# Optimization experiments

Hardware: AMD Instinct MI355X
Metric: run time of the kernel (lower is better)

## Reference

```python
import jax, jax.numpy as jnp
import numpy as np

IN_F = (16, 16, 16)
OUT_F = (16, 16, 16)
RANKS = (8, 8, 8, 8, 8, 8)


def setup_inputs() -> dict:
    key = jax.random.key(0)
    ks = jax.random.split(key, 9)
    x = jax.random.normal(ks[0], (4096, int(np.prod(IN_F))), dtype=jnp.float32)
    # core ~ U[0,1)*0.1 as in torch.rand(ranks)*0.1
    core = jax.random.uniform(ks[1], RANKS, dtype=jnp.float32) * 0.1
    # factor matrices: 3 out-side (out_f[i], r[i]) then 3 in-side (in_f[i], r[i+3])
    shapes = [(OUT_F[i], RANKS[i]) for i in range(3)] + [(IN_F[i], RANKS[i + 3]) for i in range(3)]
    f0, f1, f2, f3, f4, f5 = [
        jax.random.normal(ks[2 + i], shapes[i], dtype=jnp.float32) * 0.1 for i in range(6)
    ]
    bias = jnp.zeros((int(np.prod(OUT_F)),), dtype=jnp.float32)
    return {"x": x, "core": core, "f0": f0, "f1": f1, "f2": f2,
            "f3": f3, "f4": f4, "f5": f5, "bias": bias}


def reference(x, core, f0, f1, f2, f3, f4, f5, bias):
    # x: [N, prod(IN_F)] -> [N, i1, i2, i3]
    xr = x.reshape(-1, *IN_F)
    # Reconstruct full dense weight from Tucker factors (faithful to original)
    # core: [r0..r5]; f0..f2 out-side (out_dim, r); f3..f5 in-side (in_dim, r)
    W = jnp.einsum('ijklmn,ai,bj,ck,dl,em,fn->abcdef', core, f0, f1, f2, f3, f4, f5)
    # Contract input with in-side modes: [N, o1, o2, o3]
    res = jnp.einsum('abcdef,ndef->nabc', W, xr)
    y = res.reshape(-1, int(np.prod(OUT_F)))
    return y + bias
```

## Files before the change

kernel.cpp:

```cpp
#include <hip/hip_runtime.h>

#define THREADS 256

typedef __attribute__((ext_vector_type(8))) short bf16x8;
typedef __attribute__((ext_vector_type(4))) float f32x4;

__device__ inline unsigned short f2bf(float f) {
    union { float f; unsigned int u; } v; v.f = f;
    unsigned int r = v.u + 0x7fffu + ((v.u >> 16) & 1u);
    return (unsigned short)(r >> 16);
}

__global__ __launch_bounds__(THREADS) void k_in_contract(
    const float* __restrict__ x,
    const float* __restrict__ f3, const float* __restrict__ f4,
    const float* __restrict__ f5,
    unsigned short* __restrict__ u3b, int N)
{
    const int n = blockIdx.x;
    const int t = threadIdx.x;

    __shared__ float fs[256];
    __shared__ float u1s[256 * 9];
    __shared__ float u2s[128 * 9];

    if (t < 128) { fs[t] = f3[t]; fs[128 + t] = f4[t]; }

    float xv[16];
    {
        const float4* xr = (const float4*)(x + (size_t)n * 4096 + t * 16);
        float4 a0 = xr[0], a1 = xr[1], a2 = xr[2], a3 = xr[3];
        xv[0]=a0.x; xv[1]=a0.y; xv[2]=a0.z; xv[3]=a0.w;
        xv[4]=a1.x; xv[5]=a1.y; xv[6]=a1.z; xv[7]=a1.w;
        xv[8]=a2.x; xv[9]=a2.y; xv[10]=a2.z; xv[11]=a2.w;
        xv[12]=a3.x; xv[13]=a3.y; xv[14]=a3.z; xv[15]=a3.w;
    }

    float acc8[8];
    #pragma unroll
    for (int q = 0; q < 8; ++q) acc8[q] = 0.f;
    #pragma unroll
    for (int f = 0; f < 16; ++f) {
        const float xf = xv[f];
        #pragma unroll
        for (int n6 = 0; n6 < 8; ++n6)
            acc8[n6] = fmaf(xf, f5[f*8 + n6], acc8[n6]);
    }
    __syncthreads();
    #pragma unroll
    for (int n6 = 0; n6 < 8; ++n6) u1s[t*9 + n6] = acc8[n6];
    __syncthreads();

    {
        const int d = t >> 4, m = (t >> 1) & 7, h = t & 1;
        float fr[16];
        #pragma unroll
        for (int e = 0; e < 16; ++e) fr[e] = fs[128 + e*8 + m];
        float a4[4] = {0.f, 0.f, 0.f, 0.f};
        #pragma unroll
        for (int e = 0; e < 16; ++e) {
            const int base = (d*16 + e)*9 + h*4;
            #pragma unroll
            for (int q = 0; q < 4; ++q)
                a4[q] = fmaf(u1s[base + q], fr[e], a4[q]);
        }
        #pragma unroll
        for (int q = 0; q < 4; ++q) u2s[(d*8 + m)*9 + h*4 + q] = a4[q];
    }
    __syncthreads();

    {
        const int l = t >> 5, m = (t >> 2) & 7, h = t & 3;
        float fr[16];
        #pragma unroll
        for (int d = 0; d < 16; ++d) fr[d] = fs[d*8 + l];
        float a2[2] = {0.f, 0.f};
        #pragma unroll
        for (int d = 0; d < 16; ++d) {
            const int base = (d*8 + m)*9 + h*2;
            a2[0] = fmaf(u2s[base],     fr[d], a2[0]);
            a2[1] = fmaf(u2s[base + 1], fr[d], a2[1]);
        }
        unsigned int pk = (unsigned int)f2bf(a2[0]) |
                          ((unsigned int)f2bf(a2[1]) << 16);
        ((unsigned int*)u3b)[(size_t)n * 256 + t] = pk;
    }
}

__global__ __launch_bounds__(THREADS) void k_convert_core(
    const float* __restrict__ core, unsigned short* __restrict__ coreb)
{
    const int i = blockIdx.x * THREADS + threadIdx.x;
    float4 c = ((const float4*)core)[i];
    ushort4 o;
    o.x = f2bf(c.x); o.y = f2bf(c.y); o.z = f2bf(c.z); o.w = f2bf(c.w);
    ((ushort4*)coreb)[i] = o;
}

__global__ __launch_bounds__(THREADS) void k_core_gemm_mfma(
    const unsigned short* __restrict__ u3b,
    const unsigned short* __restrict__ coreb,
    float* __restrict__ v, int N)
{
    const int t    = threadIdx.x;
    const int lane = t & 63;
    const int wave = t >> 6;
    const int m0 = blockIdx.x * 128 + wave * 32;
    const int p0 = blockIdx.y * 32;
    const int lr = lane & 15;
    const int lq = lane >> 4;

    const unsigned short* aptr0 = u3b   + (size_t)(m0 + lr) * 512 + lq * 8;
    const unsigned short* aptr1 = aptr0 + 16 * 512;
    const unsigned short* bptr0 = coreb + (size_t)(p0 + lr) * 512 + lq * 8;
    const unsigned short* bptr1 = bptr0 + 16 * 512;

    f32x4 acc00 = {0.f,0.f,0.f,0.f}, acc01 = {0.f,0.f,0.f,0.f};
    f32x4 acc10 = {0.f,0.f,0.f,0.f}, acc11 = {0.f,0.f,0.f,0.f};

    #pragma unroll
    for (int k0 = 0; k0 < 512; k0 += 32) {
        bf16x8 a0 = *(const bf16x8*)(aptr0 + k0);
        bf16x8 a1 = *(const bf16x8*)(aptr1 + k0);
        bf16x8 b0 = *(const bf16x8*)(bptr0 + k0);
        bf16x8 b1 = *(const bf16x8*)(bptr1 + k0);
        acc00 = __builtin_amdgcn_mfma_f32_16x16x32_bf16(a0, b0, acc00, 0, 0, 0);
        acc01 = __builtin_amdgcn_mfma_f32_16x16x32_bf16(a0, b1, acc01, 0, 0, 0);
        acc10 = __builtin_amdgcn_mfma_f32_16x16x32_bf16(a1, b0, acc10, 0, 0, 0);
        acc11 = __builtin_amdgcn_mfma_f32_16x16x32_bf16(a1, b1, acc11, 0, 0, 0);
    }

    const int row = m0 + lq * 4;
    const int col = p0 + lr;
    #pragma unroll
    for (int r = 0; r < 4; ++r) {
        v[(size_t)(row + r) * 512 + col]           = acc00[r];
        v[(size_t)(row + r) * 512 + col + 16]      = acc01[r];
        v[(size_t)(row + 16 + r) * 512 + col]      = acc10[r];
        v[(size_t)(row + 16 + r) * 512 + col + 16] = acc11[r];
    }
}

__global__ __launch_bounds__(THREADS) void k_out_expand(
    const float* __restrict__ v,
    const float* __restrict__ f0, const float* __restrict__ f1,
    const float* __restrict__ f2, const float* __restrict__ bias,
    float* __restrict__ y, int N)
{
    const int n = blockIdx.x;
    const int t = threadIdx.x;

    __shared__ float fs[256];
    __shared__ float vs[512];
    __shared__ float w1s[128 * 9];
    __shared__ float w2s[256 * 9];

    if (t < 128) { fs[t] = f0[t]; fs[128 + t] = f1[t]; }
    if (t < 128) ((float4*)vs)[t] = ((const float4*)(v + (size_t)n*512))[t];
    __syncthreads();

    {
        const int a = t >> 4, j = (t >> 1) & 7, h = t & 1;
        float fr[8];
        #pragma unroll
        for (int i = 0; i < 8; ++i) fr[i] = fs[a*8 + i];
        float a4[4] = {0.f, 0.f, 0.f, 0.f};
        #pragma unroll
        for (int i = 0; i < 8; ++i) {
            const int base = i*64 + j*8 + h*4;
            #pragma unroll
            for (int q = 0; q < 4; ++q)
                a4[q] = fmaf(vs[base + q], fr[i], a4[q]);
        }
        #pragma unroll
        for (int q = 0; q < 4; ++q) w1s[(a*8 + j)*9 + h*4 + q] = a4[q];
    }
    __syncthreads();

    {
        const int a = t >> 4, b = t & 15;
        float fr[8];
        #pragma unroll
        for (int j = 0; j < 8; ++j) fr[j] = fs[128 + b*8 + j];
        float a8[8] = {0.f,0.f,0.f,0.f,0.f,0.f,0.f,0.f};
        #pragma unroll
        for (int j = 0; j < 8; ++j) {
            const int base = (a*8 + j)*9;
            const float fj = fr[j];
            #pragma unroll
            for (int k = 0; k < 8; ++k)
                a8[k] = fmaf(w1s[base + k], fj, a8[k]);
        }
        #pragma unroll
        for (int k = 0; k < 8; ++k) w2s[(a*16 + b)*9 + k] = a8[k];
    }
    __syncthreads();

    {
        const int a = t >> 4, b = t & 15;
        float wr[8];
        #pragma unroll
        for (int k = 0; k < 8; ++k) wr[k] = w2s[(a*16 + b)*9 + k];

        const int obase = a*256 + b*16;
        float4 b4[4];
        {
            const float4* bp = (const float4*)(bias + obase);
            b4[0] = bp[0]; b4[1] = bp[1]; b4[2] = bp[2]; b4[3] = bp[3];
        }
        float yv[16];
        #pragma unroll
        for (int q = 0; q < 4; ++q) {
            yv[q*4+0] = b4[q].x; yv[q*4+1] = b4[q].y;
            yv[q*4+2] = b4[q].z; yv[q*4+3] = b4[q].w;
        }
        #pragma unroll
        for (int c = 0; c < 16; ++c) {
            float s = yv[c];
            #pragma unroll
            for (int k = 0; k < 8; ++k)
                s = fmaf(wr[k], f2[c*8 + k], s);
            yv[c] = s;
        }
        float4* o = (float4*)(y + (size_t)n*4096 + obase);
        #pragma unroll
        for (int q = 0; q < 4; ++q)
            o[q] = make_float4(yv[q*4+0], yv[q*4+1], yv[q*4+2], yv[q*4+3]);
    }
}

extern "C" void kernel_launch(void* const* d_in, const int* in_sizes, int n_in,
                              void* d_out, int out_size, void* d_ws, size_t ws_size,
                              hipStream_t stream)
{
    const float* x    = (const float*)d_in[0];
    const float* core = (const float*)d_in[1];
    const float* f0   = (const float*)d_in[2];
    const float* f1   = (const float*)d_in[3];
    const float* f2   = (const float*)d_in[4];
    const float* f3   = (const float*)d_in[5];
    const float* f4   = (const float*)d_in[6];
    const float* f5   = (const float*)d_in[7];
    const float* bias = (const float*)d_in[8];
    float* y = (float*)d_out;

    const int N = in_sizes[0] / 4096;

    unsigned short* u3b   = (unsigned short*)d_ws;
    unsigned short* coreb = u3b + (size_t)N * 512;
    float*          v     = (float*)(coreb + 512 * 512);

    k_in_contract<<<N, THREADS, 0, stream>>>(x, f3, f4, f5, u3b, N);
    k_convert_core<<<256, THREADS, 0, stream>>>(core, coreb);
    dim3 gb(N / 128, 512 / 32);
    k_core_gemm_mfma<<<gb, THREADS, 0, stream>>>(u3b, coreb, v, N);
    k_out_expand<<<N, THREADS, 0, stream>>>(v, f0, f1, f2, bias, y, N);
}
```

Before: 163.3 us.

## Fuse core MFMA GEMM with output expansion through LDS

Merges the core-tensor GEMM and the output-side factor expansion into one kernel. Each block computes 16 rows of v with MFMA and keeps them in padded LDS, then expands them row by row into y with a double-buffered w1 scratch. This removes the global round trip of the v intermediate and one kernel launch. In exchange there are only N/16 blocks, and each block re-reads the full core matrix from global or L2, which may increase B-operand traffic and reduce parallelism.

```diff
diff --git a/kernel.cpp b/kernel.cpp
--- a/kernel.cpp
+++ b/kernel.cpp
@@ -9,6 +9,12 @@
     union { float f; unsigned int u; } v; v.f = f;
     unsigned int r = v.u + 0x7fffu + ((v.u >> 16) & 1u);
     return (unsigned short)(r >> 16);
+}
+
+__device__ inline void lds_barrier() {
+    asm volatile("s_waitcnt lgkmcnt(0)" ::: "memory");
+    __builtin_amdgcn_s_barrier();
+    asm volatile("" ::: "memory");
 }
 
 __global__ __launch_bounds__(THREADS) void k_in_contract(
@@ -97,135 +103,127 @@
     ((ushort4*)coreb)[i] = o;
 }
 
-__global__ __launch_bounds__(THREADS) void k_core_gemm_mfma(
+#define GE_THREADS 512
+#define VSTRIDE 516
+
+__global__ __launch_bounds__(GE_THREADS) void k_gemm_expand(
     const unsigned short* __restrict__ u3b,
     const unsigned short* __restrict__ coreb,
-    float* __restrict__ v, int N)
-{
-    const int t    = threadIdx.x;
-    const int lane = t & 63;
-    const int wave = t >> 6;
-    const int m0 = blockIdx.x * 128 + wave * 32;
-    const int p0 = blockIdx.y * 32;
-    const int lr = lane & 15;
-    const int lq = lane >> 4;
-
-    const unsigned short* aptr0 = u3b   + (size_t)(m0 + lr) * 512 + lq * 8;
-    const unsigned short* aptr1 = aptr0 + 16 * 512;
-    const unsigned short* bptr0 = coreb + (size_t)(p0 + lr) * 512 + lq * 8;
-    const unsigned short* bptr1 = bptr0 + 16 * 512;
-
-    f32x4 acc00 = {0.f,0.f,0.f,0.f}, acc01 = {0.f,0.f,0.f,0.f};
-    f32x4 acc10 = {0.f,0.f,0.f,0.f}, acc11 = {0.f,0.f,0.f,0.f};
-
-    #pragma unroll
-    for (int k0 = 0; k0 < 512; k0 += 32) {
-        bf16x8 a0 = *(const bf16x8*)(aptr0 + k0);
-        bf16x8 a1 = *(const bf16x8*)(aptr1 + k0);
-        bf16x8 b0 = *(const bf16x8*)(bptr0 + k0);
-        bf16x8 b1 = *(const bf16x8*)(bptr1 + k0);
-        acc00 = __builtin_amdgcn_mfma_f32_16x16x32_bf16(a0, b0, acc00, 0, 0, 0);
-        acc01 = __builtin_amdgcn_mfma_f32_16x16x32_bf16(a0, b1, acc01, 0, 0, 0);
-        acc10 = __builtin_amdgcn_mfma_f32_16x16x32_bf16(a1, b0, acc10, 0, 0, 0);
-        acc11 = __builtin_amdgcn_mfma_f32_16x16x32_bf16(a1, b1, acc11, 0, 0, 0);
-    }
-
-    const int row = m0 + lq * 4;
-    const int col = p0 + lr;
-    #pragma unroll
-    for (int r = 0; r < 4; ++r) {
-        v[(size_t)(row + r) * 512 + col]           = acc00[r];
-        v[(size_t)(row + r) * 512 + col + 16]      = acc01[r];
-        v[(size_t)(row + 16 + r) * 512 + col]      = acc10[r];
-        v[(size_t)(row + 16 + r) * 512 + col + 16] = acc11[r];
-    }
-}
-
-__global__ __launch_bounds__(THREADS) void k_out_expand(
-    const float* __restrict__ v,
     const float* __restrict__ f0, const float* __restrict__ f1,
     const float* __restrict__ f2, const float* __restrict__ bias,
     float* __restrict__ y, int N)
 {
-    const int n = blockIdx.x;
-    const int t = threadIdx.x;
+    const int t  = threadIdx.x;
+    const int n0 = blockIdx.x * 16;
+    const int tt = t & 255;
+    const int rp = t >> 8;
 
     __shared__ float fs[256];
-    __shared__ float vs[512];
-    __shared__ float w1s[128 * 9];
-    __shared__ float w2s[256 * 9];
-
-    if (t < 128) { fs[t] = f0[t]; fs[128 + t] = f1[t]; }
-    if (t < 128) ((float4*)vs)[t] = ((const float4*)(v + (size_t)n*512))[t];
-    __syncthreads();
-
-    {
-        const int a = t >> 4, j = (t >> 1) & 7, h = t & 1;
-        float fr[8];
-        #pragma unroll
-        for (int i = 0; i < 8; ++i) fr[i] = fs[a*8 + i];
-        float a4[4] = {0.f, 0.f, 0.f, 0.f};
-        #pragma unroll
-        for (int i = 0; i < 8; ++i) {
-            const int base = i*64 + j*8 + h*4;
+    __shared__ float v_lds[16 * VSTRIDE];
+    __shared__ float w1s[2 * 128 * 9];
+
+    if (t < 128) fs[t] = f0[t];
+    else if (t < 256) fs[t] = f1[t - 128];
+
+    float4 b4[4];
+    {
+        const float4* bp = (const float4*)(bias + tt * 16);
+        b4[0] = bp[0]; b4[1] = bp[1]; b4[2] = bp[2]; b4[3] = bp[3];
+    }
+
+    {
+        const int lane = t & 63;
+        const int w  = t >> 6;
+        const int lr = lane & 15;
+        const int lq = lane >> 4;
+
+        const unsigned short* ap = u3b + (size_t)(n0 + lr) * 512 + lq * 8;
+        bf16x8 a[16];
+        #pragma unroll
+        for (int kt = 0; kt < 16; ++kt)
+            a[kt] = *(const bf16x8*)(ap + kt * 32);
+
+        const unsigned short* bp0 = coreb + (size_t)(w * 64 + lr) * 512 + lq * 8;
+        f32x4 acc[4] = {{0.f,0.f,0.f,0.f},{0.f,0.f,0.f,0.f},
+                        {0.f,0.f,0.f,0.f},{0.f,0.f,0.f,0.f}};
+        #pragma unroll
+        for (int kt = 0; kt < 16; ++kt) {
+            #pragma unroll
+            for (int j = 0; j < 4; ++j) {
+                bf16x8 b = *(const bf16x8*)(bp0 + (size_t)j * 16 * 512 + kt * 32);
+                acc[j] = __builtin_amdgcn_mfma_f32_16x16x32_bf16(a[kt], b, acc[j], 0, 0, 0);
+            }
+        }
+        #pragma unroll
+        for (int j = 0; j < 4; ++j) {
+            #pragma unroll
+            for (int r = 0; r < 4; ++r)
+                v_lds[(lq*4 + r) * VSTRIDE + w*64 + j*16 + lr] = acc[j][r];
+        }
+    }
+    __syncthreads();
+
+    const int a1 = tt >> 4, j1 = (tt >> 1) & 7, h1 = tt & 1;
+    const int b2 = tt & 15;
+    float fr1[8], fr2[8];
+    #pragma unroll
+    for (int i = 0; i < 8; ++i) fr1[i] = fs[a1*8 + i];
+    #pragma unroll
+    for (int j = 0; j < 8; ++j) fr2[j] = fs[128 + b2*8 + j];
+
+    float* w1p = w1s + rp * (128 * 9);
+
+    #pragma unroll 1
+    for (int it = 0; it < 8; ++it) {
+        const int row = it * 2 + rp;
+        const float* vrow = v_lds + row * VSTRIDE;
+
+        {
+            float a4[4] = {0.f, 0.f, 0.f, 0.f};
+            #pragma unroll
+            for (int i = 0; i < 8; ++i) {
+                const int base = i*64 + j1*8 + h1*4;
+                const float fi = fr1[i];
+                #pragma unroll
+                for (int q = 0; q < 4; ++q)
+                    a4[q] = fmaf(vrow[base + q], fi, a4[q]);
+            }
             #pragma unroll
             for (int q = 0; q < 4; ++q)
-                a4[q] = fmaf(vs[base + q], fr[i], a4[q]);
-        }
-        #pragma unroll
-        for (int q = 0; q < 4; ++q) w1s[(a*8 + j)*9 + h*4 + q] = a4[q];
-    }
-    __syncthreads();
-
-    {
-        const int a = t >> 4, b = t & 15;
-        float fr[8];
-        #pragma unroll
-        for (int j = 0; j < 8; ++j) fr[j] = fs[128 + b*8 + j];
-        float a8[8] = {0.f,0.f,0.f,0.f,0.f,0.f,0.f,0.f};
-        #pragma unroll
-        for (int j = 0; j < 8; ++j) {
-            const int base = (a*8 + j)*9;
-            const float fj = fr[j];
-            #pragma unroll
-            for (int k = 0; k < 8; ++k)
-                a8[k] = fmaf(w1s[base + k], fj, a8[k]);
-        }
-        #pragma unroll
-        for (int k = 0; k < 8; ++k) w2s[(a*16 + b)*9 + k] = a8[k];
-    }
-    __syncthreads();
-
-    {
-        const int a = t >> 4, b = t & 15;
-        float wr[8];
-        #pragma unroll
-        for (int k = 0; k < 8; ++k) wr[k] = w2s[(a*16 + b)*9 + k];
-
-        const int obase = a*256 + b*16;
-        float4 b4[4];
+                w1p[(a1*8 + j1)*9 + h1*4 + q] = a4[q];
+        }
+        lds_barrier();
+
         {
-            const float4* bp = (const float4*)(bias + obase);
-            b4[0] = bp[0]; b4[1] = bp[1]; b4[2] = bp[2]; b4[3] = bp[3];
-        }
-        float yv[16];
-        #pragma unroll
-        for (int q = 0; q < 4; ++q) {
-            yv[q*4+0] = b4[q].x; yv[q*4+1] = b4[q].y;
-            yv[q*4+2] = b4[q].z; yv[q*4+3] = b4[q].w;
-        }
-        #pragma unroll
-        for (int c = 0; c < 16; ++c) {
-            float s = yv[c];
-            #pragma unroll
-            for (int k = 0; k < 8; ++k)
-                s = fmaf(wr[k], f2[c*8 + k], s);
-            yv[c] = s;
-        }
-        float4* o = (float4*)(y + (size_t)n*4096 + obase);
-        #pragma unroll
-        for (int q = 0; q < 4; ++q)
-            o[q] = make_float4(yv[q*4+0], yv[q*4+1], yv[q*4+2], yv[q*4+3]);
+            float a8[8] = {0.f,0.f,0.f,0.f,0.f,0.f,0.f,0.f};
+            #pragma unroll
+            for (int j = 0; j < 8; ++j) {
+                const int base = (a1*8 + j)*9;
+                const float fj = fr2[j];
+                #pragma unroll
+                for (int k = 0; k < 8; ++k)
+                    a8[k] = fmaf(w1p[base + k], fj, a8[k]);
+            }
+            float yv[16];
+            #pragma unroll
+            for (int q = 0; q < 4; ++q) {
+                yv[q*4+0] = b4[q].x; yv[q*4+1] = b4[q].y;
+                yv[q*4+2] = b4[q].z; yv[q*4+3] = b4[q].w;
+            }
+            #pragma unroll
+            for (int c = 0; c < 16; ++c) {
+                float s = yv[c];
+                #pragma unroll
+                for (int k = 0; k < 8; ++k)
+                    s = fmaf(a8[k], f2[c*8 + k], s);
+                yv[c] = s;
+            }
+            float4* o = (float4*)(y + (size_t)(n0 + row) * 4096 + tt * 16);
+            #pragma unroll
+            for (int q = 0; q < 4; ++q)
+                o[q] = make_float4(yv[q*4+0], yv[q*4+1], yv[q*4+2], yv[q*4+3]);
+        }
+        lds_barrier();
     }
 }
 
@@ -248,11 +246,9 @@
 
     unsigned short* u3b   = (unsigned short*)d_ws;
     unsigned short* coreb = u3b + (size_t)N * 512;
-    float*          v     = (float*)(coreb + 512 * 512);
 
     k_in_contract<<<N, THREADS, 0, stream>>>(x, f3, f4, f5, u3b, N);
     k_convert_core<<<256, THREADS, 0, stream>>>(core, coreb);
-    dim3 gb(N / 128, 512 / 32);
-    k_core_gemm_mfma<<<gb, THREADS, 0, stream>>>(u3b, coreb, v, N);
-    k_out_expand<<<N, THREADS, 0, stream>>>(v, f0, f1, f2, bias, y, N);
-}
+    k_gemm_expand<<<N / 16, GE_THREADS, 0, stream>>>(u3b, coreb, f0, f1, f2,
+                                                     bias, y, N);
+}
```

New measurement: 162.1 us. About the same (-0.7%).

## Retile core GEMM into smaller blocks and give each wave its own output-expand row

Applied to the files above, without the earlier changes.

The core GEMM now has each wave compute a single 16x16 tile, with blocks of 16 rows by 64 columns. This launches many more blocks, trading register reuse for occupancy. The output-expansion kernel now handles four samples per block, one per wave. It replaces block-wide __syncthreads with per-wave LDS waits and keeps the intermediate products in registers. This removes block barriers and shrinks the grid, at the cost of higher register pressure (a 64-float array per thread) and uncoalesced per-thread reads of the factor matrices from global memory.

```diff
diff --git a/kernel.cpp b/kernel.cpp
--- a/kernel.cpp
+++ b/kernel.cpp
@@ -97,7 +97,7 @@
     ((ushort4*)coreb)[i] = o;
 }
 
-__global__ __launch_bounds__(THREADS) void k_core_gemm_mfma(
+__global__ __launch_bounds__(THREADS, 8) void k_core_gemm2(
     const unsigned short* __restrict__ u3b,
     const unsigned short* __restrict__ coreb,
     float* __restrict__ v, int N)
@@ -105,127 +105,119 @@
     const int t    = threadIdx.x;
     const int lane = t & 63;
     const int wave = t >> 6;
-    const int m0 = blockIdx.x * 128 + wave * 32;
-    const int p0 = blockIdx.y * 32;
+    const int m0 = blockIdx.x * 16;
+    const int p0 = blockIdx.y * 64 + wave * 16;
     const int lr = lane & 15;
     const int lq = lane >> 4;
 
-    const unsigned short* aptr0 = u3b   + (size_t)(m0 + lr) * 512 + lq * 8;
-    const unsigned short* aptr1 = aptr0 + 16 * 512;
-    const unsigned short* bptr0 = coreb + (size_t)(p0 + lr) * 512 + lq * 8;
-    const unsigned short* bptr1 = bptr0 + 16 * 512;
-
-    f32x4 acc00 = {0.f,0.f,0.f,0.f}, acc01 = {0.f,0.f,0.f,0.f};
-    f32x4 acc10 = {0.f,0.f,0.f,0.f}, acc11 = {0.f,0.f,0.f,0.f};
-
-    #pragma unroll
-    for (int k0 = 0; k0 < 512; k0 += 32) {
-        bf16x8 a0 = *(const bf16x8*)(aptr0 + k0);
-        bf16x8 a1 = *(const bf16x8*)(aptr1 + k0);
-        bf16x8 b0 = *(const bf16x8*)(bptr0 + k0);
-        bf16x8 b1 = *(const bf16x8*)(bptr1 + k0);
-        acc00 = __builtin_amdgcn_mfma_f32_16x16x32_bf16(a0, b0, acc00, 0, 0, 0);
-        acc01 = __builtin_amdgcn_mfma_f32_16x16x32_bf16(a0, b1, acc01, 0, 0, 0);
-        acc10 = __builtin_amdgcn_mfma_f32_16x16x32_bf16(a1, b0, acc10, 0, 0, 0);
-        acc11 = __builtin_amdgcn_mfma_f32_16x16x32_bf16(a1, b1, acc11, 0, 0, 0);
+    const unsigned short* ap = u3b   + (size_t)(m0 + lr) * 512 + lq * 8;
+    const unsigned short* bp = coreb + (size_t)(p0 + lr) * 512 + lq * 8;
+
+    f32x4 acc = {0.f, 0.f, 0.f, 0.f};
+    #pragma unroll
+    for (int kt = 0; kt < 16; ++kt) {
+        bf16x8 a = *(const bf16x8*)(ap + kt * 32);
+        bf16x8 b = *(const bf16x8*)(bp + kt * 32);
+        acc = __builtin_amdgcn_mfma_f32_16x16x32_bf16(a, b, acc, 0, 0, 0);
     }
 
     const int row = m0 + lq * 4;
     const int col = p0 + lr;
     #pragma unroll
-    for (int r = 0; r < 4; ++r) {
-        v[(size_t)(row + r) * 512 + col]           = acc00[r];
-        v[(size_t)(row + r) * 512 + col + 16]      = acc01[r];
-        v[(size_t)(row + 16 + r) * 512 + col]      = acc10[r];
-        v[(size_t)(row + 16 + r) * 512 + col + 16] = acc11[r];
-    }
-}
-
-__global__ __launch_bounds__(THREADS) void k_out_expand(
+    for (int r = 0; r < 4; ++r)
+        v[(size_t)(row + r) * 512 + col] = acc[r];
+}
+
+#define EXW 4
+
+__global__ __launch_bounds__(THREADS, 4) void k_out_expand2(
     const float* __restrict__ v,
     const float* __restrict__ f0, const float* __restrict__ f1,
     const float* __restrict__ f2, const float* __restrict__ bias,
     float* __restrict__ y, int N)
 {
-    const int n = blockIdx.x;
-    const int t = threadIdx.x;
-
-    __shared__ float fs[256];
-    __shared__ float vs[512];
-    __shared__ float w1s[128 * 9];
-    __shared__ float w2s[256 * 9];
-
-    if (t < 128) { fs[t] = f0[t]; fs[128 + t] = f1[t]; }
-    if (t < 128) ((float4*)vs)[t] = ((const float4*)(v + (size_t)n*512))[t];
-    __syncthreads();
-
-    {
-        const int a = t >> 4, j = (t >> 1) & 7, h = t & 1;
+    const int t    = threadIdx.x;
+    const int wave = t >> 6;
+    const int lane = t & 63;
+    const int row  = blockIdx.x * EXW + wave;
+    const int a = lane >> 2;
+    const int s = lane & 3;
+
+    __shared__ float vs[EXW][512];
+    __shared__ float w1s[EXW][16 * 68];
+
+    {
+        const float4* vp = (const float4*)(v + (size_t)row * 512);
+        float4 v0 = vp[lane * 2];
+        float4 v1 = vp[lane * 2 + 1];
+        float4* d = (float4*)&vs[wave][lane * 8];
+        d[0] = v0; d[1] = v1;
+    }
+    asm volatile("s_waitcnt lgkmcnt(0)" ::: "memory");
+    __builtin_amdgcn_sched_barrier(0);
+
+    {
         float fr[8];
         #pragma unroll
-        for (int i = 0; i < 8; ++i) fr[i] = fs[a*8 + i];
-        float a4[4] = {0.f, 0.f, 0.f, 0.f};
-        #pragma unroll
-        for (int i = 0; i < 8; ++i) {
-            const int base = i*64 + j*8 + h*4;
-            #pragma unroll
-            for (int q = 0; q < 4; ++q)
-                a4[q] = fmaf(vs[base + q], fr[i], a4[q]);
-        }
-        #pragma unroll
-        for (int q = 0; q < 4; ++q) w1s[(a*8 + j)*9 + h*4 + q] = a4[q];
-    }
-    __syncthreads();
-
-    {
-        const int a = t >> 4, b = t & 15;
-        float fr[8];
-        #pragma unroll
-        for (int j = 0; j < 8; ++j) fr[j] = fs[128 + b*8 + j];
-        float a8[8] = {0.f,0.f,0.f,0.f,0.f,0.f,0.f,0.f};
-        #pragma unroll
-        for (int j = 0; j < 8; ++j) {
-            const int base = (a*8 + j)*9;
-            const float fj = fr[j];
-            #pragma unroll
-            for (int k = 0; k < 8; ++k)
-                a8[k] = fmaf(w1s[base + k], fj, a8[k]);
-        }
-        #pragma unroll
-        for (int k = 0; k < 8; ++k) w2s[(a*16 + b)*9 + k] = a8[k];
-    }
-    __syncthreads();
-
-    {
-        const int a = t >> 4, b = t & 15;
-        float wr[8];
-        #pragma unroll
-        for (int k = 0; k < 8; ++k) wr[k] = w2s[(a*16 + b)*9 + k];
-
-        const int obase = a*256 + b*16;
-        float4 b4[4];
-        {
-            const float4* bp = (const float4*)(bias + obase);
-            b4[0] = bp[0]; b4[1] = bp[1]; b4[2] = bp[2]; b4[3] = bp[3];
-        }
-        float yv[16];
-        #pragma unroll
-        for (int q = 0; q < 4; ++q) {
-            yv[q*4+0] = b4[q].x; yv[q*4+1] = b4[q].y;
-            yv[q*4+2] = b4[q].z; yv[q*4+3] = b4[q].w;
-        }
-        #pragma unroll
-        for (int c = 0; c < 16; ++c) {
-            float s = yv[c];
-            #pragma unroll
-            for (int k = 0; k < 8; ++k)
-                s = fmaf(wr[k], f2[c*8 + k], s);
-            yv[c] = s;
-        }
-        float4* o = (float4*)(y + (size_t)n*4096 + obase);
-        #pragma unroll
-        for (int q = 0; q < 4; ++q)
-            o[q] = make_float4(yv[q*4+0], yv[q*4+1], yv[q*4+2], yv[q*4+3]);
+        for (int i = 0; i < 8; ++i) fr[i] = f0[a * 8 + i];
+        #pragma unroll
+        for (int cmb = 0; cmb < 4; ++cmb) {
+            const int idx = cmb * 4 + s;
+            float ax = 0.f, ay = 0.f, az = 0.f, aw = 0.f;
+            #pragma unroll
+            for (int i = 0; i < 8; ++i) {
+                float4 vv = *(const float4*)&vs[wave][i * 64 + idx * 4];
+                const float fi = fr[i];
+                ax = fmaf(vv.x, fi, ax); ay = fmaf(vv.y, fi, ay);
+                az = fmaf(vv.z, fi, az); aw = fmaf(vv.w, fi, aw);
+            }
+            *(float4*)&w1s[wave][a * 68 + idx * 4] = make_float4(ax, ay, az, aw);
+        }
+    }
+    asm volatile("s_waitcnt lgkmcnt(0)" ::: "memory");
+    __builtin_amdgcn_sched_barrier(0);
+
+    {
+        float w1r[64];
+        #pragma unroll
+        for (int m = 0; m < 16; ++m) {
+            float4 q = *(const float4*)&w1s[wave][a * 68 + m * 4];
+            w1r[m*4+0] = q.x; w1r[m*4+1] = q.y;
+            w1r[m*4+2] = q.z; w1r[m*4+3] = q.w;
+        }
+        #pragma unroll
+        for (int s2 = 0; s2 < 4; ++s2) {
+            const int b = s2 * 4 + s;
+            float fb[8];
+            #pragma unroll
+            for (int j = 0; j < 8; ++j) fb[j] = f1[b * 8 + j];
+
+            float w2[8] = {0.f,0.f,0.f,0.f,0.f,0.f,0.f,0.f};
+            #pragma unroll
+            for (int j = 0; j < 8; ++j) {
+                const float fj = fb[j];
+                #pragma unroll
+                for (int k = 0; k < 8; ++k)
+                    w2[k] = fmaf(w1r[j * 8 + k], fj, w2[k]);
+            }
+
+            const int ob = a * 256 + b * 16;
+            const float4* bp4 = (const float4*)(bias + ob);
+            float4* op = (float4*)(y + (size_t)row * 4096 + ob);
+            #pragma unroll
+            for (int cq = 0; cq < 4; ++cq) {
+                float4 bb = bp4[cq];
+                float r0 = bb.x, r1 = bb.y, r2 = bb.z, r3 = bb.w;
+                #pragma unroll
+                for (int k = 0; k < 8; ++k) {
+                    r0 = fmaf(w2[k], f2[(cq*4 + 0) * 8 + k], r0);
+                    r1 = fmaf(w2[k], f2[(cq*4 + 1) * 8 + k], r1);
+                    r2 = fmaf(w2[k], f2[(cq*4 + 2) * 8 + k], r2);
+                    r3 = fmaf(w2[k], f2[(cq*4 + 3) * 8 + k], r3);
+                }
+                op[cq] = make_float4(r0, r1, r2, r3);
+            }
+        }
     }
 }
 
@@ -252,7 +244,7 @@
 
     k_in_contract<<<N, THREADS, 0, stream>>>(x, f3, f4, f5, u3b, N);
     k_convert_core<<<256, THREADS, 0, stream>>>(core, coreb);
-    dim3 gb(N / 128, 512 / 32);
-    k_core_gemm_mfma<<<gb, THREADS, 0, stream>>>(u3b, coreb, v, N);
-    k_out_expand<<<N, THREADS, 0, stream>>>(v, f0, f1, f2, bias, y, N);
-}
+    dim3 gb(N / 16, 512 / 64);
+    k_core_gemm2<<<gb, THREADS, 0, stream>>>(u3b, coreb, v, N);
+    k_out_expand2<<<N / EXW, THREADS, 0, stream>>>(v, f0, f1, f2, bias, y, N);
+}
```

Measured after the change: 178.0 us. 9.0% more time.

## Restructure input contraction to one wave per row and fuse core conversion

Applied to the files above, without the earlier changes.

Rewrites the input-side mode contraction so that each wave handles a whole sample row. The first two mode contractions are held in registers with shuffle reductions, and only one per-wave LDS round trip is used, with no block barriers. The separate core bf16 conversion kernel is folded into the first 256 blocks of this kernel, which removes one launch. Each thread now holds 64 accumulators under a 4-blocks-per-CU launch bound, which risks register spills, and each lane reads 64 floats, so global x reads may coalesce less well.

```diff
diff --git a/kernel.cpp b/kernel.cpp
--- a/kernel.cpp
+++ b/kernel.cpp
@@ -11,90 +11,101 @@
     return (unsigned short)(r >> 16);
 }
 
-__global__ __launch_bounds__(THREADS) void k_in_contract(
+__global__ __launch_bounds__(THREADS, 4) void k_in_contract3(
     const float* __restrict__ x,
     const float* __restrict__ f3, const float* __restrict__ f4,
-    const float* __restrict__ f5,
-    unsigned short* __restrict__ u3b, int N)
-{
-    const int n = blockIdx.x;
-    const int t = threadIdx.x;
-
-    __shared__ float fs[256];
-    __shared__ float u1s[256 * 9];
-    __shared__ float u2s[128 * 9];
-
-    if (t < 128) { fs[t] = f3[t]; fs[128 + t] = f4[t]; }
-
-    float xv[16];
-    {
-        const float4* xr = (const float4*)(x + (size_t)n * 4096 + t * 16);
-        float4 a0 = xr[0], a1 = xr[1], a2 = xr[2], a3 = xr[3];
-        xv[0]=a0.x; xv[1]=a0.y; xv[2]=a0.z; xv[3]=a0.w;
-        xv[4]=a1.x; xv[5]=a1.y; xv[6]=a1.z; xv[7]=a1.w;
-        xv[8]=a2.x; xv[9]=a2.y; xv[10]=a2.z; xv[11]=a2.w;
-        xv[12]=a3.x; xv[13]=a3.y; xv[14]=a3.z; xv[15]=a3.w;
-    }
-
-    float acc8[8];
-    #pragma unroll
-    for (int q = 0; q < 8; ++q) acc8[q] = 0.f;
-    #pragma unroll
-    for (int f = 0; f < 16; ++f) {
-        const float xf = xv[f];
-        #pragma unroll
-        for (int n6 = 0; n6 < 8; ++n6)
-            acc8[n6] = fmaf(xf, f5[f*8 + n6], acc8[n6]);
-    }
-    __syncthreads();
-    #pragma unroll
-    for (int n6 = 0; n6 < 8; ++n6) u1s[t*9 + n6] = acc8[n6];
-    __syncthreads();
-
-    {
-        const int d = t >> 4, m = (t >> 1) & 7, h = t & 1;
-        float fr[16];
-        #pragma unroll
-        for (int e = 0; e < 16; ++e) fr[e] = fs[128 + e*8 + m];
-        float a4[4] = {0.f, 0.f, 0.f, 0.f};
-        #pragma unroll
-        for (int e = 0; e < 16; ++e) {
-            const int base = (d*16 + e)*9 + h*4;
-            #pragma unroll
-            for (int q = 0; q < 4; ++q)
-                a4[q] = fmaf(u1s[base + q], fr[e], a4[q]);
-        }
-        #pragma unroll
-        for (int q = 0; q < 4; ++q) u2s[(d*8 + m)*9 + h*4 + q] = a4[q];
-    }
-    __syncthreads();
-
-    {
-        const int l = t >> 5, m = (t >> 2) & 7, h = t & 3;
-        float fr[16];
-        #pragma unroll
-        for (int d = 0; d < 16; ++d) fr[d] = fs[d*8 + l];
-        float a2[2] = {0.f, 0.f};
+    const float* __restrict__ f5, const float* __restrict__ core,
+    unsigned short* __restrict__ u3b, unsigned short* __restrict__ coreb,
+    int N)
+{
+    const int t    = threadIdx.x;
+    const int wave = t >> 6;
+    const int lane = t & 63;
+    const int row  = blockIdx.x * 4 + wave;
+    const int a = lane >> 2;
+    const int b = lane & 3;
+
+    __shared__ float u2s[4][16 * 68];
+
+    if (blockIdx.x < 256) {
+        const int i = blockIdx.x * THREADS + t;
+        float4 c = ((const float4*)core)[i];
+        ushort4 o;
+        o.x = f2bf(c.x); o.y = f2bf(c.y); o.z = f2bf(c.z); o.w = f2bf(c.w);
+        ((ushort4*)coreb)[i] = o;
+    }
+
+    const float* xr = x + (size_t)row * 4096 + lane * 64;
+
+    float psum[64];
+    #pragma unroll
+    for (int i = 0; i < 64; ++i) psum[i] = 0.f;
+
+    #pragma unroll
+    for (int e0 = 0; e0 < 4; ++e0) {
+        float4 x0 = ((const float4*)xr)[e0*4 + 0];
+        float4 x1 = ((const float4*)xr)[e0*4 + 1];
+        float4 x2 = ((const float4*)xr)[e0*4 + 2];
+        float4 x3 = ((const float4*)xr)[e0*4 + 3];
+        float xc[16] = {x0.x,x0.y,x0.z,x0.w, x1.x,x1.y,x1.z,x1.w,
+                        x2.x,x2.y,x2.z,x2.w, x3.x,x3.y,x3.z,x3.w};
+
+        float u1[8] = {0.f,0.f,0.f,0.f,0.f,0.f,0.f,0.f};
+        #pragma unroll
+        for (int f = 0; f < 16; ++f) {
+            const float xf = xc[f];
+            #pragma unroll
+            for (int n6 = 0; n6 < 8; ++n6)
+                u1[n6] = fmaf(xf, f5[f*8 + n6], u1[n6]);
+        }
+
+        const float4* gp = (const float4*)(f4 + (4*b + e0) * 8);
+        float4 g0 = gp[0], g1 = gp[1];
+        const float g[8] = {g0.x,g0.y,g0.z,g0.w, g1.x,g1.y,g1.z,g1.w};
+        #pragma unroll
+        for (int m = 0; m < 8; ++m) {
+            const float gm = g[m];
+            #pragma unroll
+            for (int n6 = 0; n6 < 8; ++n6)
+                psum[m*8 + n6] = fmaf(u1[n6], gm, psum[m*8 + n6]);
+        }
+    }
+
+    #pragma unroll
+    for (int i = 0; i < 64; ++i) {
+        psum[i] += __shfl_xor(psum[i], 1, 64);
+        psum[i] += __shfl_xor(psum[i], 2, 64);
+    }
+
+    {
+        float* ws = &u2s[wave][0];
+        #pragma unroll
+        for (int mm = 0; mm < 2; ++mm) {
+            const int m = 2*b + mm;
+            *(float4*)&ws[a*68 + m*8 + 0] =
+                make_float4(psum[m*8+0], psum[m*8+1], psum[m*8+2], psum[m*8+3]);
+            *(float4*)&ws[a*68 + m*8 + 4] =
+                make_float4(psum[m*8+4], psum[m*8+5], psum[m*8+6], psum[m*8+7]);
+        }
+    }
+    asm volatile("s_waitcnt lgkmcnt(0)" ::: "memory");
+    __builtin_amdgcn_sched_barrier(0);
+
+    {
+        const float* ws = &u2s[wave][0];
+        float acc[8] = {0.f,0.f,0.f,0.f,0.f,0.f,0.f,0.f};
         #pragma unroll
         for (int d = 0; d < 16; ++d) {
-            const int base = (d*8 + m)*9 + h*2;
-            a2[0] = fmaf(u2s[base],     fr[d], a2[0]);
-            a2[1] = fmaf(u2s[base + 1], fr[d], a2[1]);
-        }
-        unsigned int pk = (unsigned int)f2bf(a2[0]) |
-                          ((unsigned int)f2bf(a2[1]) << 16);
-        ((unsigned int*)u3b)[(size_t)n * 256 + t] = pk;
-    }
-}
-
-__global__ __launch_bounds__(THREADS) void k_convert_core(
-    const float* __restrict__ core, unsigned short* __restrict__ coreb)
-{
-    const int i = blockIdx.x * THREADS + threadIdx.x;
-    float4 c = ((const float4*)core)[i];
-    ushort4 o;
-    o.x = f2bf(c.x); o.y = f2bf(c.y); o.z = f2bf(c.z); o.w = f2bf(c.w);
-    ((ushort4*)coreb)[i] = o;
+            const float u2v = ws[d*68 + lane];
+            #pragma unroll
+            for (int l = 0; l < 8; ++l)
+                acc[l] = fmaf(u2v, f3[d*8 + l], acc[l]);
+        }
+        unsigned short* orow = u3b + (size_t)row * 512;
+        #pragma unroll
+        for (int l = 0; l < 8; ++l)
+            orow[l*64 + lane] = f2bf(acc[l]);
+    }
 }
 
 __global__ __launch_bounds__(THREADS) void k_core_gemm_mfma(
@@ -250,8 +261,8 @@
     unsigned short* coreb = u3b + (size_t)N * 512;
     float*          v     = (float*)(coreb + 512 * 512);
 
-    k_in_contract<<<N, THREADS, 0, stream>>>(x, f3, f4, f5, u3b, N);
-    k_convert_core<<<256, THREADS, 0, stream>>>(core, coreb);
+    k_in_contract3<<<N / 4, THREADS, 0, stream>>>(x, f3, f4, f5, core,
+                                                  u3b, coreb, N);
     dim3 gb(N / 128, 512 / 32);
     k_core_gemm_mfma<<<gb, THREADS, 0, stream>>>(u3b, coreb, v, N);
     k_out_expand<<<N, THREADS, 0, stream>>>(v, f0, f1, f2, bias, y, N);
```

Result: slower. 227.5 us (+39.3%).
